# Optimization experiments

Hardware: AMD Instinct MI355X
Metric: run time of the kernel (lower is better)

## Reference

```python
import jax, jax.numpy as jnp
import numpy as np
from jax import lax

B, N, D = 2, 2048, 256
S, DC, E = 16, 4, 2
DI = E * D            # d_inner = 512
DTR = (D + 15) // 16  # dt_rank = 16


def layernorm(x, w, b):
    m = x.mean(-1, keepdims=True)
    v = ((x - m) ** 2).mean(-1, keepdims=True)
    return (x - m) / jnp.sqrt(v + 1e-5) * w + b


def mamba_block(x, in_w, conv_w, conv_b, xproj_w, dt_w, dt_b, A_log, Dp, out_w):
    # x: [B, N, D]
    xz = jnp.einsum('bnd,ed->bne', x, in_w)          # [B,N,2*DI]
    xc, z = jnp.split(xz, 2, axis=-1)
    # depthwise causal conv1d, kernel DC, left-pad DC-1
    xpad = jnp.pad(xc, ((0, 0), (DC - 1, 0), (0, 0)))
    xconv = sum(xpad[:, k:k + N, :] * conv_w[:, k] for k in range(DC)) + conv_b
    xa = jax.nn.silu(xconv)                           # [B,N,DI]
    x_dbl = jnp.einsum('bnd,ed->bne', xa, xproj_w)    # [B,N,DTR+2S]
    dt = x_dbl[..., :DTR]
    Bm = x_dbl[..., DTR:DTR + S]                      # [B,N,S]
    Cm = x_dbl[..., DTR + S:]                         # [B,N,S]
    dt = jax.nn.softplus(jnp.einsum('bnr,dr->bnd', dt, dt_w) + dt_b)  # [B,N,DI]
    A = -jnp.exp(A_log)                               # [DI,S]
    dA = jnp.exp(dt[..., None] * A)                   # [B,N,DI,S]
    dBu = dt[..., None] * Bm[:, :, None, :] * xa[..., None]

    def step(h, inp):
        dA_t, dBu_t, C_t = inp
        h = dA_t * h + dBu_t                          # [B,DI,S]
        y = jnp.einsum('bds,bs->bd', h, C_t)
        return h, y

    h0 = jnp.zeros((x.shape[0], DI, S), dtype=x.dtype)
    _, ys = lax.scan(step, h0, (dA.transpose(1, 0, 2, 3), dBu.transpose(1, 0, 2, 3), Cm.transpose(1, 0, 2)))
    y = ys.transpose(1, 0, 2) + xa * Dp               # skip D*u
    y = y * jax.nn.silu(z)
    return jnp.einsum('bnd,ed->bne', y, out_w)        # [B,N,D]


def stream_fwd(x, nw, nb, in_w, conv_w, conv_b, xproj_w, dt_w, dt_b, A_log, Dp, out_w):
    return x + mamba_block(layernorm(x, nw, nb), in_w, conv_w, conv_b, xproj_w, dt_w, dt_b, A_log, Dp, out_w)


def setup_inputs() -> dict:
    key = jax.random.key(0)
    ks = jax.random.split(key, 24)
    s = 0.02
    inp = {
        'edge_features': jax.random.normal(ks[0], (B, N, D), jnp.float32),
        'blob_features': jax.random.normal(ks[1], (B, N, D), jnp.float32),
        'spectral_features': jax.random.normal(ks[2], (B, N, D), jnp.float32),
        'norm_w': jnp.ones((3, D)),
        'norm_b': jnp.zeros((3, D)),
        'in_w': jax.random.normal(ks[3], (3, 2 * DI, D)) * s,
        'conv_w': jax.random.normal(ks[4], (3, DI, DC)) * s,
        'conv_b': jnp.zeros((3, DI)),
        'xproj_w': jax.random.normal(ks[5], (3, DTR + 2 * S, DI)) * s,
        'dt_w': jax.random.normal(ks[6], (3, DI, DTR)) * s,
        'dt_b': jax.random.uniform(ks[7], (3, DI), minval=-4.0, maxval=-2.0),
        'A_log': jnp.tile(jnp.log(jnp.arange(1, S + 1, dtype=jnp.float32)), (3, DI, 1)),
        'Dp': jnp.ones((3, DI)),
        'out_w': jax.random.normal(ks[8], (3, D, DI)) * s,
        'temperature': jnp.ones((1,)) * 0.1,
        'agg_w1': jax.random.normal(ks[9], (D, 3 * D)) * s,
        'agg_b1': jnp.zeros((D,)),
        'agg_w2': jax.random.normal(ks[10], (3, D)) * s,
        'agg_b2': jnp.zeros((3,)),
        'proj_w': jax.random.normal(ks[11], (D, 3 * D)) * s,
        'proj_b': jnp.zeros((D,)),
    }
    return inp


def reference(edge_features, blob_features, spectral_features, norm_w, norm_b, in_w,
              conv_w, conv_b, xproj_w, dt_w, dt_b, A_log, Dp, out_w, temperature,
              agg_w1, agg_b1, agg_w2, agg_b2, proj_w, proj_b):
    streams = jnp.stack([edge_features, blob_features, spectral_features])  # [3,B,N,D]
    proc = jax.vmap(stream_fwd)(streams, norm_w, norm_b, in_w, conv_w, conv_b,
                                xproj_w, dt_w, dt_b, A_log, Dp, out_w)      # [3,B,N,D]
    edge_p, blob_p, spec_p = proc[0], proc[1], proc[2]
    multi = jnp.concatenate([edge_p, blob_p, spec_p], axis=-1)              # [B,N,3D]
    pooled = multi.mean(axis=1, keepdims=True)                              # [B,1,3D]
    h = jax.nn.gelu(jnp.einsum('bne,de->bnd', pooled, agg_w1) + agg_b1)
    coeffs = jax.nn.softmax(jnp.einsum('bnd,kd->bnk', h, agg_w2) + agg_b2, axis=-1)
    coeffs = jax.nn.softmax(coeffs / (temperature + 1e-6), axis=-1)         # [B,1,3]
    weighted = (coeffs[:, :, 0:1] * edge_p + coeffs[:, :, 1:2] * blob_p +
                coeffs[:, :, 2:3] * spec_p)
    out = jnp.einsum('bne,de->bnd', multi, proj_w) + proj_b + weighted
    return out  # dropout is identity in eval
```

## Files before the change

kernel.cpp:

```cpp
#include <hip/hip_runtime.h>
#include <hip/hip_bf16.h>

#define NB 2
#define NN 2048
#define ND 256
#define NS 16
#define NDC 4
#define NDI 512
#define NDTR 16
#define LCH 32
#define NCH 64

typedef __hip_bfloat16 bf16;
typedef __attribute__((ext_vector_type(8))) __bf16 bf16x8;
typedef __attribute__((ext_vector_type(4))) float f32x4;

__device__ __forceinline__ float b2f(bf16 h) { return __bfloat162float(h); }

__device__ __forceinline__ void dec8(const uint4 u, float w[8]) {
    union { unsigned u; float f; } c;
    c.u = u.x << 16;          w[0] = c.f;
    c.u = u.x & 0xffff0000u;  w[1] = c.f;
    c.u = u.y << 16;          w[2] = c.f;
    c.u = u.y & 0xffff0000u;  w[3] = c.f;
    c.u = u.z << 16;          w[4] = c.f;
    c.u = u.z & 0xffff0000u;  w[5] = c.f;
    c.u = u.w << 16;          w[6] = c.f;
    c.u = u.w & 0xffff0000u;  w[7] = c.f;
}

struct CvtArgs { const void* s[21]; };
__device__ __constant__ const int seg_cum[22] = {
    0, 1048576, 2097152, 3145728, 3146496, 3147264, 3933696, 3939840,
    3941376, 4015104, 4039680, 4041216, 4065792, 4067328, 4460544, 4460545,
    4657153, 4657409, 4658177, 4658180, 4854788, 4855044 };
__device__ __constant__ const int seg_dst[21] = {
    0,        1048576,  2097152,  4847616, 4848384, 3145728, 4841472, 4849152, 4325376,
    4399104,  4850688,  4423680,  4852224, 3932160, 4855056, 4448256, 4853760, 4854016,
    4854784,  4644864,  4854800 };

__global__ __launch_bounds__(256) void k_convert(CvtArgs a, int* __restrict__ flag,
                                                 bf16* __restrict__ dst,
                                                 float* __restrict__ pooled)
{
    int idx = blockIdx.x * 256 + threadIdx.x;
    unsigned v0 = ((const unsigned*)a.s[3])[0];
    int f = ((v0 & 0xFFFFu) == 0u) ? 1 : 0;
    if (idx == 0) flag[0] = f;
    if (idx < 1536) pooled[idx] = 0.0f;
    if (idx >= 4855044) return;
    int seg = 0;
    #pragma unroll
    for (int i = 1; i < 21; i++) if (idx >= seg_cum[i]) seg = i;
    int off = idx - seg_cum[seg];
    bf16 v;
    if (f) v = __float2bfloat16(((const float*)a.s[seg])[off]);
    else   v = ((const bf16*)a.s[seg])[off];
    dst[seg_dst[seg] + off] = v;
}

__global__ __launch_bounds__(256) void k_layernorm(
    const bf16* __restrict__ e, const bf16* __restrict__ bl, const bf16* __restrict__ sp,
    const bf16* __restrict__ nw, const bf16* __restrict__ nb, bf16* __restrict__ xn)
{
    int row = blockIdx.x;
    int sb = row >> 11, n = row & (NN - 1);
    int s = sb >> 1, b = sb & 1;
    const bf16* xin = (s == 0) ? e : ((s == 1) ? bl : sp);
    int t = threadIdx.x;
    float v = b2f(xin[((b << 11) + n) * ND + t]);
    float s1 = v, s2 = v * v;
    #pragma unroll
    for (int m = 1; m < 64; m <<= 1) { s1 += __shfl_xor(s1, m); s2 += __shfl_xor(s2, m); }
    __shared__ float r1[4], r2[4];
    int w = t >> 6;
    if ((t & 63) == 0) { r1[w] = s1; r2[w] = s2; }
    __syncthreads();
    float mean = (r1[0] + r1[1] + r1[2] + r1[3]) * (1.0f / ND);
    float ms   = (r2[0] + r2[1] + r2[2] + r2[3]) * (1.0f / ND);
    float inv = rsqrtf(ms - mean * mean + 1e-5f);
    float wv = b2f(nw[s * ND + t]), bv = b2f(nb[s * ND + t]);
    xn[row * ND + t] = __float2bfloat16((v - mean) * inv * wv + bv);
}

__global__ __launch_bounds__(256) void k_inproj_t(
    const bf16* __restrict__ xn, const bf16* __restrict__ in_w,
    bf16* __restrict__ xc, bf16* __restrict__ z)
{
    __shared__ bf16 As[128 * 72];
    __shared__ bf16 Bs[128 * 72];
    int bid = blockIdx.x;
    int bm = bid >> 3, bn = bid & 7;
    int m0 = bm * 128, e0 = bn * 128;
    int s = m0 >> 12;
    const bf16* W = in_w + (size_t)s * (2 * NDI) * ND;
    int t = threadIdx.x;
    int w = t >> 6, l = t & 63;
    int wm = w >> 1, wn = w & 1;
    int quad = l >> 4, lan = l & 15;
    f32x4 acc[4][4];
    #pragma unroll
    for (int mi = 0; mi < 4; mi++)
        #pragma unroll
        for (int j = 0; j < 4; j++) acc[mi][j] = (f32x4){0.f, 0.f, 0.f, 0.f};
    for (int kc0 = 0; kc0 < 256; kc0 += 64) {
        __syncthreads();
        #pragma unroll
        for (int i = 0; i < 4; i++) {
            int li = i * 256 + t;
            int row = li >> 3, col = (li & 7) * 8;
            *(uint4*)&As[row * 72 + col] =
                *(const uint4*)(xn + (size_t)(m0 + row) * ND + kc0 + col);
        }
        #pragma unroll
        for (int i = 0; i < 4; i++) {
            int li = i * 256 + t;
            int row = li >> 3, col = (li & 7) * 8;
            *(uint4*)&Bs[row * 72 + col] =
                *(const uint4*)(W + (size_t)(e0 + row) * ND + kc0 + col);
        }
        __syncthreads();
        #pragma unroll
        for (int kc = 0; kc < 64; kc += 32) {
            bf16x8 af[4], bf[4];
            #pragma unroll
            for (int mi = 0; mi < 4; mi++)
                af[mi] = *(const bf16x8*)&As[(wm * 64 + mi * 16 + lan) * 72 + kc + quad * 8];
            #pragma unroll
            for (int j = 0; j < 4; j++)
                bf[j] = *(const bf16x8*)&Bs[(wn * 64 + j * 16 + lan) * 72 + kc + quad * 8];
            #pragma unroll
            for (int mi = 0; mi < 4; mi++)
                #pragma unroll
                for (int j = 0; j < 4; j++)
                    acc[mi][j] = __builtin_amdgcn_mfma_f32_16x16x32_bf16(af[mi], bf[j], acc[mi][j], 0, 0, 0);
        }
    }
    #pragma unroll
    for (int mi = 0; mi < 4; mi++) {
        #pragma unroll
        for (int j = 0; j < 4; j++) {
            int e = e0 + wn * 64 + j * 16 + lan;
            bf16* dst = (e < NDI) ? xc : z;
            int ec = e & (NDI - 1);
            #pragma unroll
            for (int r = 0; r < 4; r++) {
                int m = m0 + wm * 64 + mi * 16 + quad * 4 + r;
                dst[(size_t)m * NDI + ec] = __float2bfloat16(acc[mi][j][r]);
            }
        }
    }
}

__global__ __launch_bounds__(256) void k_conv(
    const bf16* __restrict__ xc, const bf16* __restrict__ conv_w,
    const bf16* __restrict__ conv_b, bf16* __restrict__ xa)
{
    int idx = blockIdx.x * 256 + threadIdx.x;
    int d8 = (idx & 63) * 8;
    int rn = idx >> 6;
    int n = rn & (NN - 1);
    int sb = rn >> 11;
    int s = sb >> 1;
    const uint4* cwp = (const uint4*)(conv_w + ((size_t)s * NDI + d8) * NDC);
    float cwf[32];
    dec8(cwp[0], cwf); dec8(cwp[1], cwf + 8); dec8(cwp[2], cwf + 16); dec8(cwp[3], cwf + 24);
    float bias[8];
    dec8(*(const uint4*)(conv_b + (size_t)s * NDI + d8), bias);
    size_t g = (size_t)rn * NDI + d8;
    float xv[4][8];
    #pragma unroll
    for (int tau = 0; tau < 4; tau++) {
        if (n >= tau) dec8(*(const uint4*)(xc + g - (size_t)tau * NDI), xv[tau]);
        else
            #pragma unroll
            for (int j = 0; j < 8; j++) xv[tau][j] = 0.0f;
    }
    union { bf16 h[8]; uint4 u; } o;
    #pragma unroll
    for (int j = 0; j < 8; j++) {
        float a = bias[j];
        #pragma unroll
        for (int k = 0; k < 4; k++) a += cwf[j * 4 + k] * xv[3 - k][j];
        a = a / (1.0f + __expf(-a));
        o.h[j] = __float2bfloat16(a);
    }
    *(uint4*)(xa + g) = o.u;
}

__global__ __launch_bounds__(256) void k_xproj_t(
    const bf16* __restrict__ xa, const bf16* __restrict__ xproj_w,
    float* __restrict__ xpart)
{
    __shared__ bf16 As[64 * 72];
    __shared__ bf16 Bs[48 * 72];
    int bid = blockIdx.x;
    int bm = bid >> 2, ks = bid & 3;
    int m0 = bm * 64;
    int s = m0 >> 12;
    const bf16* W = xproj_w + (size_t)s * 48 * NDI;
    int t = threadIdx.x;
    int w = t >> 6, l = t & 63;
    int quad = l >> 4, lan = l & 15;
    f32x4 acc[3];
    #pragma unroll
    for (int j = 0; j < 3; j++) acc[j] = (f32x4){0.f, 0.f, 0.f, 0.f};
    for (int kc0 = ks * 128; kc0 < ks * 128 + 128; kc0 += 64) {
        __syncthreads();
        #pragma unroll
        for (int i = 0; i < 2; i++) {
            int li = i * 256 + t;
            int row = li >> 3, col = (li & 7) * 8;
            *(uint4*)&As[row * 72 + col] =
                *(const uint4*)(xa + (size_t)(m0 + row) * NDI + kc0 + col);
        }
        {
            int li = t;
            if (li < 384) {
                int row = li >> 3, col = (li & 7) * 8;
                *(uint4*)&Bs[row * 72 + col] =
                    *(const uint4*)(W + (size_t)row * NDI + kc0 + col);
            }
            int li2 = 256 + t;
            if (li2 < 384) {
                int row = li2 >> 3, col = (li2 & 7) * 8;
                *(uint4*)&Bs[row * 72 + col] =
                    *(const uint4*)(W + (size_t)row * NDI + kc0 + col);
            }
        }
        __syncthreads();
        #pragma unroll
        for (int kc = 0; kc < 64; kc += 32) {
            bf16x8 af = *(const bf16x8*)&As[(w * 16 + lan) * 72 + kc + quad * 8];
            #pragma unroll
            for (int j = 0; j < 3; j++) {
                bf16x8 bf = *(const bf16x8*)&Bs[(j * 16 + lan) * 72 + kc + quad * 8];
                acc[j] = __builtin_amdgcn_mfma_f32_16x16x32_bf16(af, bf, acc[j], 0, 0, 0);
            }
        }
    }
    float* dst = xpart + (size_t)ks * (12288 * 48);
    #pragma unroll
    for (int j = 0; j < 3; j++) {
        int e = j * 16 + lan;
        #pragma unroll
        for (int r = 0; r < 4; r++) {
            int m = m0 + w * 16 + quad * 4 + r;
            dst[(size_t)m * 48 + e] = acc[j][r];
        }
    }
}

__global__ __launch_bounds__(256) void k_dt2(
    const float* __restrict__ xpart, const bf16* __restrict__ dt_w,
    const bf16* __restrict__ dt_b, float* __restrict__ xdbl, bf16* __restrict__ dt)
{
    __shared__ float xs[4][48];
    int row0 = blockIdx.x * 4;
    int s = row0 >> 12;
    int t = threadIdx.x;
    if (t < 192) {
        int r = t / 48, e = t % 48;
        size_t base = (size_t)(row0 + r) * 48 + e;
        const size_t seg = (size_t)12288 * 48;
        float v = xpart[base] + xpart[base + seg] + xpart[base + 2 * seg] + xpart[base + 3 * seg];
        xs[r][e] = v;
        if (e >= 16) xdbl[base] = v;
    }
    __syncthreads();
    #pragma unroll
    for (int dd = 0; dd < 2; dd++) {
        int d = t + dd * 256;
        const uint4* wp = (const uint4*)(dt_w + ((size_t)s * NDI + d) * NDTR);
        float w[16]; dec8(wp[0], w); dec8(wp[1], w + 8);
        float bias = b2f(dt_b[s * NDI + d]);
        #pragma unroll
        for (int r = 0; r < 4; r++) {
            float a = bias;
            #pragma unroll
            for (int j = 0; j < 16; j++) a += w[j] * xs[r][j];
            a = (a > 20.0f) ? a : log1pf(__expf(a));
            dt[(size_t)(row0 + r) * NDI + d] = __float2bfloat16(a);
        }
    }
}

__global__ __launch_bounds__(256) void k_scan1(
    const bf16* __restrict__ dt, const bf16* __restrict__ xa,
    const bf16* __restrict__ A_log, const float* __restrict__ xdbl,
    float* __restrict__ Hend, float* __restrict__ Pprod)
{
    __shared__ float Bs[LCH * NS];
    int bid = blockIdx.x;
    int sb = bid / (NCH * 2);
    int rem = bid % (NCH * 2);
    int chunk = rem >> 1, dg = rem & 1;
    int s = sb >> 1;
    int t = threadIdx.x;
    int d = dg * 256 + t;
    int n0 = chunk * LCH;
    size_t rowbase = (size_t)sb * NN;
    if (t < 128) {
        int row = t >> 2, q = t & 3;
        ((float4*)Bs)[t] = ((const float4*)(xdbl + (rowbase + n0 + row) * 48 + 16))[q];
    }
    float A[16];
    {
        const uint4* ap = (const uint4*)(A_log + ((size_t)s * NDI + d) * NS);
        float al[8]; dec8(ap[0], al);
        #pragma unroll
        for (int i = 0; i < 8; i++) A[i] = -__expf(al[i]);
        dec8(ap[1], al);
        #pragma unroll
        for (int i = 0; i < 8; i++) A[8 + i] = -__expf(al[i]);
    }
    __syncthreads();
    float h[16], P[16];
    #pragma unroll
    for (int i = 0; i < 16; i++) { h[i] = 0.0f; P[i] = 1.0f; }
    const bf16* dtp = dt + (rowbase + n0) * NDI + d;
    const bf16* xap = xa + (rowbase + n0) * NDI + d;
    for (int nl = 0; nl < LCH; nl += 4) {
        float dtv[4], xav[4];
        #pragma unroll
        for (int j = 0; j < 4; j++) {
            dtv[j] = b2f(dtp[(size_t)(nl + j) * NDI]);
            xav[j] = b2f(xap[(size_t)(nl + j) * NDI]);
        }
        #pragma unroll
        for (int j = 0; j < 4; j++) {
            float bcom = dtv[j] * xav[j];
            const float4* br = (const float4*)&Bs[(nl + j) * NS];
            float4 b0 = br[0], b1 = br[1], b2 = br[2], b3 = br[3];
            float bv[16] = {b0.x,b0.y,b0.z,b0.w,b1.x,b1.y,b1.z,b1.w,
                            b2.x,b2.y,b2.z,b2.w,b3.x,b3.y,b3.z,b3.w};
            #pragma unroll
            for (int st = 0; st < 16; st++) {
                float dA = __expf(dtv[j] * A[st]);
                h[st] = dA * h[st] + bcom * bv[st];
                P[st] *= dA;
            }
        }
    }
    size_t base = ((size_t)(chunk * 6 + sb) * NS) * NDI + d;
    #pragma unroll
    for (int st = 0; st < 16; st++) {
        Hend[base + (size_t)st * NDI] = h[st];
        Pprod[base + (size_t)st * NDI] = P[st];
    }
}

__global__ __launch_bounds__(256) void k_scomb(float* __restrict__ Hend, const float* __restrict__ Pprod)
{
    int idx = blockIdx.x * 256 + threadIdx.x;
    int sb = idx >> 13;
    int rem = idx & 8191;
    int st = rem >> 9, d = rem & 511;
    float h = 0.0f;
    const size_t stride = (size_t)6 * NS * NDI;
    size_t g = ((size_t)sb * NS + st) * NDI + d;
    #pragma unroll 4
    for (int c = 0; c < NCH; c++) {
        float He = Hend[g], Pp = Pprod[g];
        Hend[g] = h;
        h = He + Pp * h;
        g += stride;
    }
}

__global__ __launch_bounds__(256) void k_scan2(
    const bf16* __restrict__ dt, const bf16* __restrict__ xa, const bf16* __restrict__ z,
    const float* __restrict__ xdbl,
    const bf16* __restrict__ A_log, const bf16* __restrict__ Dp,
    const float* __restrict__ Hstart, bf16* __restrict__ y)
{
    __shared__ float Bs[LCH * NS], Cs[LCH * NS];
    int bid = blockIdx.x;
    int sb = bid / (NCH * 2);
    int rem = bid % (NCH * 2);
    int chunk = rem >> 1, dg = rem & 1;
    int s = sb >> 1;
    int t = threadIdx.x;
    int d = dg * 256 + t;
    int n0 = chunk * LCH;
    size_t rowbase = (size_t)sb * NN;
    if (t < 128) {
        int row = t >> 2, q = t & 3;
        ((float4*)Bs)[t] = ((const float4*)(xdbl + (rowbase + n0 + row) * 48 + 16))[q];
    } else {
        int t2 = t - 128;
        int row = t2 >> 2, q = t2 & 3;
        ((float4*)Cs)[t2] = ((const float4*)(xdbl + (rowbase + n0 + row) * 48 + 32))[q];
    }
    float A[16];
    {
        const uint4* ap = (const uint4*)(A_log + ((size_t)s * NDI + d) * NS);
        float al[8]; dec8(ap[0], al);
        #pragma unroll
        for (int i = 0; i < 8; i++) A[i] = -__expf(al[i]);
        dec8(ap[1], al);
        #pragma unroll
        for (int i = 0; i < 8; i++) A[8 + i] = -__expf(al[i]);
    }
    float Dpv = b2f(Dp[s * NDI + d]);
    float h[16];
    {
        size_t base = ((size_t)(chunk * 6 + sb) * NS) * NDI + d;
        #pragma unroll
        for (int st = 0; st < 16; st++) h[st] = Hstart[base + (size_t)st * NDI];
    }
    __syncthreads();
    const bf16* dtp = dt + (rowbase + n0) * NDI + d;
    const bf16* xap = xa + (rowbase + n0) * NDI + d;
    const bf16* zp  = z  + (rowbase + n0) * NDI + d;
    bf16* yp = y + (rowbase + n0) * NDI + d;
    for (int nl = 0; nl < LCH; nl += 4) {
        float dtv[4], xav[4], zv[4];
        #pragma unroll
        for (int j = 0; j < 4; j++) {
            dtv[j] = b2f(dtp[(size_t)(nl + j) * NDI]);
            xav[j] = b2f(xap[(size_t)(nl + j) * NDI]);
            zv[j]  = b2f(zp [(size_t)(nl + j) * NDI]);
        }
        #pragma unroll
        for (int j = 0; j < 4; j++) {
            float bcom = dtv[j] * xav[j];
            const float4* br = (const float4*)&Bs[(nl + j) * NS];
            const float4* cr = (const float4*)&Cs[(nl + j) * NS];
            float4 b0 = br[0], b1 = br[1], b2 = br[2], b3 = br[3];
            float4 c0 = cr[0], c1 = cr[1], c2 = cr[2], c3 = cr[3];
            float bv[16] = {b0.x,b0.y,b0.z,b0.w,b1.x,b1.y,b1.z,b1.w,
                            b2.x,b2.y,b2.z,b2.w,b3.x,b3.y,b3.z,b3.w};
            float cv[16] = {c0.x,c0.y,c0.z,c0.w,c1.x,c1.y,c1.z,c1.w,
                            c2.x,c2.y,c2.z,c2.w,c3.x,c3.y,c3.z,c3.w};
            float yacc = 0.0f;
            #pragma unroll
            for (int st = 0; st < 16; st++) {
                float dA = __expf(dtv[j] * A[st]);
                h[st] = dA * h[st] + bcom * bv[st];
                yacc += h[st] * cv[st];
            }
            float yv = yacc + xav[j] * Dpv;
            float zz = zv[j];
            yv *= zz / (1.0f + __expf(-zz));
            yp[(size_t)(nl + j) * NDI] = __float2bfloat16(yv);
        }
    }
}

__global__ __launch_bounds__(256) void k_outproj_t(
    const bf16* __restrict__ y, const bf16* __restrict__ out_w,
    const bf16* __restrict__ e_, const bf16* __restrict__ bl, const bf16* __restrict__ sp,
    bf16* __restrict__ proc, float* __restrict__ pooled)
{
    __shared__ bf16 As[128 * 72];
    __shared__ bf16 Bs[64 * 72];
    __shared__ float colsum[64];
    int bid = blockIdx.x;
    int bm = bid >> 2, bn = bid & 3;
    int m0 = bm * 128, e0 = bn * 64;
    int s = m0 >> 12;
    const bf16* W = out_w + (size_t)s * ND * NDI;
    int t = threadIdx.x;
    int w = t >> 6, l = t & 63;
    int quad = l >> 4, lan = l & 15;
    f32x4 acc[2][4];
    #pragma unroll
    for (int mi = 0; mi < 2; mi++)
        #pragma unroll
        for (int j = 0; j < 4; j++) acc[mi][j] = (f32x4){0.f, 0.f, 0.f, 0.f};
    for (int kc0 = 0; kc0 < 512; kc0 += 64) {
        __syncthreads();
        #pragma unroll
        for (int i = 0; i < 4; i++) {
            int li = i * 256 + t;
            int row = li >> 3, col = (li & 7) * 8;
            *(uint4*)&As[row * 72 + col] =
                *(const uint4*)(y + (size_t)(m0 + row) * NDI + kc0 + col);
        }
        #pragma unroll
        for (int i = 0; i < 2; i++) {
            int li = i * 256 + t;
            int row = li >> 3, col = (li & 7) * 8;
            *(uint4*)&Bs[row * 72 + col] =
                *(const uint4*)(W + (size_t)(e0 + row) * NDI + kc0 + col);
        }
        __syncthreads();
        #pragma unroll
        for (int kc = 0; kc < 64; kc += 32) {
            bf16x8 af[2], bf[4];
            #pragma unroll
            for (int mi = 0; mi < 2; mi++)
                af[mi] = *(const bf16x8*)&As[(w * 32 + mi * 16 + lan) * 72 + kc + quad * 8];
            #pragma unroll
            for (int j = 0; j < 4; j++)
                bf[j] = *(const bf16x8*)&Bs[(j * 16 + lan) * 72 + kc + quad * 8];
            #pragma unroll
            for (int mi = 0; mi < 2; mi++)
                #pragma unroll
                for (int j = 0; j < 4; j++)
                    acc[mi][j] = __builtin_amdgcn_mfma_f32_16x16x32_bf16(af[mi], bf[j], acc[mi][j], 0, 0, 0);
        }
    }
    if (t < 64) colsum[t] = 0.0f;
    __syncthreads();
    const bf16* xin = (s == 0) ? e_ : ((s == 1) ? bl : sp);
    int b = (m0 >> 11) & 1;
    #pragma unroll
    for (int mi = 0; mi < 2; mi++) {
        #pragma unroll
        for (int j = 0; j < 4; j++) {
            int e = e0 + j * 16 + lan;
            float ps = 0.0f;
            #pragma unroll
            for (int r = 0; r < 4; r++) {
                int m = m0 + w * 32 + mi * 16 + quad * 4 + r;
                int n = m & (NN - 1);
                float v = acc[mi][j][r] + b2f(xin[((size_t)(b * NN + n)) * ND + e]);
                proc[(size_t)m * ND + e] = __float2bfloat16(v);
                ps += v;
            }
            atomicAdd(&colsum[j * 16 + lan], ps);
        }
    }
    __syncthreads();
    if (t < 64) atomicAdd(&pooled[b * 768 + s * 256 + e0 + t], colsum[t]);
}

__global__ __launch_bounds__(256) void k_coeff(
    const float* __restrict__ pooled,
    const bf16* __restrict__ agg_w1, const bf16* __restrict__ agg_b1,
    const bf16* __restrict__ agg_w2, const bf16* __restrict__ agg_b2,
    const bf16* __restrict__ temp, float* __restrict__ coeffs)
{
    __shared__ float hb[256];
    __shared__ float lg[3];
    int t = threadIdx.x;
    for (int b = 0; b < NB; b++) {
        float dot = 0.0f;
        const uint4* wp = (const uint4*)(agg_w1 + (size_t)t * 768);
        for (int k8 = 0; k8 < 96; k8++) {
            float w[8]; dec8(wp[k8], w);
            const float* pp = pooled + b * 768 + k8 * 8;
            #pragma unroll
            for (int j = 0; j < 8; j++) dot += w[j] * pp[j];
        }
        float x = b2f(agg_b1[t]) + dot * (1.0f / NN);
        float inner = 0.7978845608028654f * (x + 0.044715f * x * x * x);
        hb[t] = 0.5f * x * (1.0f + tanhf(inner));
        __syncthreads();
        if (t < 3) {
            float l = b2f(agg_b2[t]);
            const bf16* w2 = agg_w2 + t * 256;
            for (int d2 = 0; d2 < 256; d2++) l += b2f(w2[d2]) * hb[d2];
            lg[t] = l;
        }
        __syncthreads();
        if (t == 0) {
            float m = fmaxf(lg[0], fmaxf(lg[1], lg[2]));
            float e0 = __expf(lg[0] - m), e1 = __expf(lg[1] - m), e2 = __expf(lg[2] - m);
            float iS = 1.0f / (e0 + e1 + e2);
            float c0 = e0 * iS, c1 = e1 * iS, c2 = e2 * iS;
            float tt = b2f(temp[0]) + 1e-6f;
            float m2 = fmaxf(c0, fmaxf(c1, c2)) / tt;
            e0 = __expf(c0 / tt - m2); e1 = __expf(c1 / tt - m2); e2 = __expf(c2 / tt - m2);
            iS = 1.0f / (e0 + e1 + e2);
            coeffs[b * 3 + 0] = e0 * iS;
            coeffs[b * 3 + 1] = e1 * iS;
            coeffs[b * 3 + 2] = e2 * iS;
        }
        __syncthreads();
    }
}

__global__ __launch_bounds__(256) void k_final_t(
    const bf16* __restrict__ proc, const bf16* __restrict__ proj_w,
    const bf16* __restrict__ proj_b, const float* __restrict__ coeffs,
    const int* __restrict__ flag, void* __restrict__ out)
{
    __shared__ bf16 As[128 * 72];
    __shared__ bf16 Bs[64 * 72];
    int bid = blockIdx.x;
    int bm = bid >> 2, bn = bid & 3;
    int m0 = bm * 128, e0 = bn * 64;
    int b = m0 >> 11;
    int nbase = m0 & (NN - 1);
    int t = threadIdx.x;
    int w = t >> 6, l = t & 63;
    int quad = l >> 4, lan = l & 15;
    f32x4 acc[2][4];
    #pragma unroll
    for (int mi = 0; mi < 2; mi++)
        #pragma unroll
        for (int j = 0; j < 4; j++) acc[mi][j] = (f32x4){0.f, 0.f, 0.f, 0.f};
    for (int kc0 = 0; kc0 < 768; kc0 += 64) {
        int sA = kc0 >> 8, kd0 = kc0 & 255;
        const bf16* Asrc = proc + ((size_t)(sA * NB + b) * NN + nbase) * ND + kd0;
        __syncthreads();
        #pragma unroll
        for (int i = 0; i < 4; i++) {
            int li = i * 256 + t;
            int row = li >> 3, col = (li & 7) * 8;
            *(uint4*)&As[row * 72 + col] = *(const uint4*)(Asrc + (size_t)row * ND + col);
        }
        #pragma unroll
        for (int i = 0; i < 2; i++) {
            int li = i * 256 + t;
            int row = li >> 3, col = (li & 7) * 8;
            *(uint4*)&Bs[row * 72 + col] =
                *(const uint4*)(proj_w + (size_t)(e0 + row) * 768 + kc0 + col);
        }
        __syncthreads();
        #pragma unroll
        for (int kc = 0; kc < 64; kc += 32) {
            bf16x8 af[2], bf[4];
            #pragma unroll
            for (int mi = 0; mi < 2; mi++)
                af[mi] = *(const bf16x8*)&As[(w * 32 + mi * 16 + lan) * 72 + kc + quad * 8];
            #pragma unroll
            for (int j = 0; j < 4; j++)
                bf[j] = *(const bf16x8*)&Bs[(j * 16 + lan) * 72 + kc + quad * 8];
            #pragma unroll
            for (int mi = 0; mi < 2; mi++)
                #pragma unroll
                for (int j = 0; j < 4; j++)
                    acc[mi][j] = __builtin_amdgcn_mfma_f32_16x16x32_bf16(af[mi], bf[j], acc[mi][j], 0, 0, 0);
        }
    }
    float c0 = coeffs[b * 3], c1 = coeffs[b * 3 + 1], c2 = coeffs[b * 3 + 2];
    int f = flag[0];
    #pragma unroll
    for (int mi = 0; mi < 2; mi++) {
        #pragma unroll
        for (int j = 0; j < 4; j++) {
            int e = e0 + j * 16 + lan;
            float pb = b2f(proj_b[e]);
            #pragma unroll
            for (int r = 0; r < 4; r++) {
                int m = m0 + w * 32 + mi * 16 + quad * 4 + r;
                int n = m & (NN - 1);
                size_t pbase = ((size_t)b * NN + n) * ND + e;
                float wres = c0 * b2f(proc[pbase])
                           + c1 * b2f(proc[pbase + (size_t)1 * NB * NN * ND])
                           + c2 * b2f(proc[pbase + (size_t)2 * NB * NN * ND]);
                float v = acc[mi][j][r] + pb + wres;
                if (f) ((float*)out)[(size_t)m * ND + e] = v;
                else   ((bf16*)out)[(size_t)m * ND + e] = __float2bfloat16(v);
            }
        }
    }
}

extern "C" void kernel_launch(void* const* d_in, const int* in_sizes, int n_in,
                              void* d_out, int out_size, void* d_ws, size_t ws_size,
                              hipStream_t stream)
{
    char* w8 = (char*)d_ws;
    int*   flagp   = (int*)(w8);
    bf16*  cvt     = (bf16*)(w8 + 16);
    bf16*  xn      = (bf16*)(w8 + 9710160);
    bf16*  xcb     = (bf16*)(w8 + 16001616);
    bf16*  zb      = (bf16*)(w8 + 28584528);
    bf16*  xab     = (bf16*)(w8 + 41167440);
    bf16*  dtb     = (bf16*)(w8 + 53750352);
    float* xdblb   = (float*)(w8 + 66333264);
    float* pooledb = (float*)(w8 + 68692560);
    float* coeffsb = (float*)(w8 + 68698704);
    float* Hendb   = (float*)(w8 + 68698736);
    float* Pprodb  = (float*)(w8 + 81281648);
    float* xpartb  = (float*)(w8 + 93864560);
    bf16*  procb   = xn;

    const bf16* c_edge   = cvt + 0;
    const bf16* c_blob   = cvt + 1048576;
    const bf16* c_spec   = cvt + 2097152;
    const bf16* c_inw    = cvt + 3145728;
    const bf16* c_outw   = cvt + 3932160;
    const bf16* c_xpw    = cvt + 4325376;
    const bf16* c_dtw    = cvt + 4399104;
    const bf16* c_alog   = cvt + 4423680;
    const bf16* c_agg1   = cvt + 4448256;
    const bf16* c_prjw   = cvt + 4644864;
    const bf16* c_convw  = cvt + 4841472;
    const bf16* c_nrmw   = cvt + 4847616;
    const bf16* c_nrmb   = cvt + 4848384;
    const bf16* c_convb  = cvt + 4849152;
    const bf16* c_dtb    = cvt + 4850688;
    const bf16* c_dp     = cvt + 4852224;
    const bf16* c_agb1   = cvt + 4853760;
    const bf16* c_agw2   = cvt + 4854016;
    const bf16* c_agb2   = cvt + 4854784;
    const bf16* c_prjb   = cvt + 4854800;
    const bf16* c_temp   = cvt + 4855056;

    CvtArgs ca;
    for (int i = 0; i < 21; i++) ca.s[i] = d_in[i];
    k_convert<<<(4855044 + 255) / 256, 256, 0, stream>>>(ca, flagp, cvt, pooledb);

    k_layernorm<<<6 * NN, 256, 0, stream>>>(c_edge, c_blob, c_spec, c_nrmw, c_nrmb, xn);
    k_inproj_t<<<96 * 8, 256, 0, stream>>>(xn, c_inw, xcb, zb);
    k_conv<<<6 * NN * NDI / 8 / 256, 256, 0, stream>>>(xcb, c_convw, c_convb, xab);
    k_xproj_t<<<192 * 4, 256, 0, stream>>>(xab, c_xpw, xpartb);
    k_dt2<<<3072, 256, 0, stream>>>(xpartb, c_dtw, c_dtb, xdblb, dtb);
    k_scan1<<<6 * NCH * 2, 256, 0, stream>>>(dtb, xab, c_alog, xdblb, Hendb, Pprodb);
    k_scomb<<<192, 256, 0, stream>>>(Hendb, Pprodb);
    k_scan2<<<6 * NCH * 2, 256, 0, stream>>>(dtb, xab, zb, xdblb, c_alog, c_dp, Hendb, xcb);
    k_outproj_t<<<96 * 4, 256, 0, stream>>>(xcb, c_outw, c_edge, c_blob, c_spec, procb, pooledb);
    k_coeff<<<1, 256, 0, stream>>>(pooledb, c_agg1, c_agb1, c_agw2, c_agb2, c_temp, coeffsb);
    k_final_t<<<32 * 4, 256, 0, stream>>>(procb, c_prjw, c_prjb, coeffsb, flagp, d_out);
}
```

Before: 337.3 us.

## Fuse input conversion into layernorm, stage scan inputs in LDS, fold coeff into final

The three large feature tensors are no longer converted in the convert kernel. Layernorm now reads the raw inputs, writes the bf16 copy itself and reads the norm weights raw. The scan kernels stage dt, xa and z chunks in shared memory with coalesced 16-byte loads instead of strided per-thread loads. The single-block coeff kernel is folded into every block of the final GEMM, which removes one launch but makes each of the 128 blocks recompute the small MLP.

```diff
diff --git a/kernel.cpp b/kernel.cpp
--- a/kernel.cpp
+++ b/kernel.cpp
@@ -43,15 +43,16 @@
                                                  bf16* __restrict__ dst,
                                                  float* __restrict__ pooled)
 {
-    int idx = blockIdx.x * 256 + threadIdx.x;
+    int idx0 = blockIdx.x * 256 + threadIdx.x;
     unsigned v0 = ((const unsigned*)a.s[3])[0];
     int f = ((v0 & 0xFFFFu) == 0u) ? 1 : 0;
-    if (idx == 0) flag[0] = f;
-    if (idx < 1536) pooled[idx] = 0.0f;
+    if (idx0 == 0) flag[0] = f;
+    if (idx0 < 1536) pooled[idx0] = 0.0f;
+    int idx = idx0 + 3145728;
     if (idx >= 4855044) return;
-    int seg = 0;
-    #pragma unroll
-    for (int i = 1; i < 21; i++) if (idx >= seg_cum[i]) seg = i;
+    int seg = 3;
+    #pragma unroll
+    for (int i = 4; i < 21; i++) if (idx >= seg_cum[i]) seg = i;
     int off = idx - seg_cum[seg];
     bf16 v;
     if (f) v = __float2bfloat16(((const float*)a.s[seg])[off]);
@@ -59,16 +60,22 @@
     dst[seg_dst[seg] + off] = v;
 }
 
-__global__ __launch_bounds__(256) void k_layernorm(
-    const bf16* __restrict__ e, const bf16* __restrict__ bl, const bf16* __restrict__ sp,
-    const bf16* __restrict__ nw, const bf16* __restrict__ nb, bf16* __restrict__ xn)
+__global__ __launch_bounds__(256) void k_ln(
+    const void* __restrict__ e, const void* __restrict__ bl, const void* __restrict__ sp,
+    const void* __restrict__ nw_raw, const void* __restrict__ nb_raw,
+    bf16* __restrict__ cvt_in,
+    bf16* __restrict__ xn)
 {
     int row = blockIdx.x;
     int sb = row >> 11, n = row & (NN - 1);
     int s = sb >> 1, b = sb & 1;
-    const bf16* xin = (s == 0) ? e : ((s == 1) ? bl : sp);
     int t = threadIdx.x;
-    float v = b2f(xin[((b << 11) + n) * ND + t]);
+    unsigned v0 = ((const unsigned*)nw_raw)[0];
+    int f = ((v0 & 0xFFFFu) == 0u);
+    const void* xin = (s == 0) ? e : ((s == 1) ? bl : sp);
+    size_t gi = ((size_t)(b << 11) + n) * ND + t;
+    float v = f ? ((const float*)xin)[gi] : b2f(((const bf16*)xin)[gi]);
+    cvt_in[(size_t)s * 1048576 + gi] = __float2bfloat16(v);
     float s1 = v, s2 = v * v;
     #pragma unroll
     for (int m = 1; m < 64; m <<= 1) { s1 += __shfl_xor(s1, m); s2 += __shfl_xor(s2, m); }
@@ -79,8 +86,9 @@
     float mean = (r1[0] + r1[1] + r1[2] + r1[3]) * (1.0f / ND);
     float ms   = (r2[0] + r2[1] + r2[2] + r2[3]) * (1.0f / ND);
     float inv = rsqrtf(ms - mean * mean + 1e-5f);
-    float wv = b2f(nw[s * ND + t]), bv = b2f(nb[s * ND + t]);
-    xn[row * ND + t] = __float2bfloat16((v - mean) * inv * wv + bv);
+    float wv = f ? ((const float*)nw_raw)[s * ND + t] : b2f(((const bf16*)nw_raw)[s * ND + t]);
+    float bv = f ? ((const float*)nb_raw)[s * ND + t] : b2f(((const bf16*)nb_raw)[s * ND + t]);
+    xn[(size_t)row * ND + t] = __float2bfloat16((v - mean) * inv * wv + bv);
 }
 
 __global__ __launch_bounds__(256) void k_inproj_t(
@@ -290,6 +298,8 @@
     const bf16* __restrict__ A_log, const float* __restrict__ xdbl,
     float* __restrict__ Hend, float* __restrict__ Pprod)
 {
+    __shared__ bf16 dts[LCH * 256];
+    __shared__ bf16 xas[LCH * 256];
     __shared__ float Bs[LCH * NS];
     int bid = blockIdx.x;
     int sb = bid / (NCH * 2);
@@ -300,6 +310,15 @@
     int d = dg * 256 + t;
     int n0 = chunk * LCH;
     size_t rowbase = (size_t)sb * NN;
+    const bf16* dtg = dt + (rowbase + n0) * NDI + dg * 256;
+    const bf16* xag = xa + (rowbase + n0) * NDI + dg * 256;
+    #pragma unroll
+    for (int i = 0; i < 4; i++) {
+        int li = i * 256 + t;
+        int row = li >> 5, q = li & 31;
+        ((uint4*)dts)[li] = *(const uint4*)(dtg + (size_t)row * NDI + q * 8);
+        ((uint4*)xas)[li] = *(const uint4*)(xag + (size_t)row * NDI + q * 8);
+    }
     if (t < 128) {
         int row = t >> 2, q = t & 3;
         ((float4*)Bs)[t] = ((const float4*)(xdbl + (rowbase + n0 + row) * 48 + 16))[q];
@@ -318,28 +337,20 @@
     float h[16], P[16];
     #pragma unroll
     for (int i = 0; i < 16; i++) { h[i] = 0.0f; P[i] = 1.0f; }
-    const bf16* dtp = dt + (rowbase + n0) * NDI + d;
-    const bf16* xap = xa + (rowbase + n0) * NDI + d;
-    for (int nl = 0; nl < LCH; nl += 4) {
-        float dtv[4], xav[4];
-        #pragma unroll
-        for (int j = 0; j < 4; j++) {
-            dtv[j] = b2f(dtp[(size_t)(nl + j) * NDI]);
-            xav[j] = b2f(xap[(size_t)(nl + j) * NDI]);
-        }
-        #pragma unroll
-        for (int j = 0; j < 4; j++) {
-            float bcom = dtv[j] * xav[j];
-            const float4* br = (const float4*)&Bs[(nl + j) * NS];
-            float4 b0 = br[0], b1 = br[1], b2 = br[2], b3 = br[3];
-            float bv[16] = {b0.x,b0.y,b0.z,b0.w,b1.x,b1.y,b1.z,b1.w,
-                            b2.x,b2.y,b2.z,b2.w,b3.x,b3.y,b3.z,b3.w};
-            #pragma unroll
-            for (int st = 0; st < 16; st++) {
-                float dA = __expf(dtv[j] * A[st]);
-                h[st] = dA * h[st] + bcom * bv[st];
-                P[st] *= dA;
-            }
+    #pragma unroll 4
+    for (int nl = 0; nl < LCH; nl++) {
+        float dtv = b2f(dts[nl * 256 + t]);
+        float xav = b2f(xas[nl * 256 + t]);
+        float bcom = dtv * xav;
+        const float4* br = (const float4*)&Bs[nl * NS];
+        float4 b0 = br[0], b1 = br[1], b2 = br[2], b3 = br[3];
+        float bv[16] = {b0.x,b0.y,b0.z,b0.w,b1.x,b1.y,b1.z,b1.w,
+                        b2.x,b2.y,b2.z,b2.w,b3.x,b3.y,b3.z,b3.w};
+        #pragma unroll
+        for (int st = 0; st < 16; st++) {
+            float dA = __expf(dtv * A[st]);
+            h[st] = dA * h[st] + bcom * bv[st];
+            P[st] *= dA;
         }
     }
     size_t base = ((size_t)(chunk * 6 + sb) * NS) * NDI + d;
@@ -374,6 +385,9 @@
     const bf16* __restrict__ A_log, const bf16* __restrict__ Dp,
     const float* __restrict__ Hstart, bf16* __restrict__ y)
 {
+    __shared__ bf16 dts[LCH * 256];
+    __shared__ bf16 xas[LCH * 256];
+    __shared__ bf16 zs[LCH * 256];
     __shared__ float Bs[LCH * NS], Cs[LCH * NS];
     int bid = blockIdx.x;
     int sb = bid / (NCH * 2);
@@ -384,6 +398,17 @@
     int d = dg * 256 + t;
     int n0 = chunk * LCH;
     size_t rowbase = (size_t)sb * NN;
+    const bf16* dtg = dt + (rowbase + n0) * NDI + dg * 256;
+    const bf16* xag = xa + (rowbase + n0) * NDI + dg * 256;
+    const bf16* zg  = z  + (rowbase + n0) * NDI + dg * 256;
+    #pragma unroll
+    for (int i = 0; i < 4; i++) {
+        int li = i * 256 + t;
+        int row = li >> 5, q = li & 31;
+        ((uint4*)dts)[li] = *(const uint4*)(dtg + (size_t)row * NDI + q * 8);
+        ((uint4*)xas)[li] = *(const uint4*)(xag + (size_t)row * NDI + q * 8);
+        ((uint4*)zs)[li]  = *(const uint4*)(zg  + (size_t)row * NDI + q * 8);
+    }
     if (t < 128) {
         int row = t >> 2, q = t & 3;
         ((float4*)Bs)[t] = ((const float4*)(xdbl + (rowbase + n0 + row) * 48 + 16))[q];
@@ -410,41 +435,31 @@
         for (int st = 0; st < 16; st++) h[st] = Hstart[base + (size_t)st * NDI];
     }
     __syncthreads();
-    const bf16* dtp = dt + (rowbase + n0) * NDI + d;
-    const bf16* xap = xa + (rowbase + n0) * NDI + d;
-    const bf16* zp  = z  + (rowbase + n0) * NDI + d;
     bf16* yp = y + (rowbase + n0) * NDI + d;
-    for (int nl = 0; nl < LCH; nl += 4) {
-        float dtv[4], xav[4], zv[4];
-        #pragma unroll
-        for (int j = 0; j < 4; j++) {
-            dtv[j] = b2f(dtp[(size_t)(nl + j) * NDI]);
-            xav[j] = b2f(xap[(size_t)(nl + j) * NDI]);
-            zv[j]  = b2f(zp [(size_t)(nl + j) * NDI]);
-        }
-        #pragma unroll
-        for (int j = 0; j < 4; j++) {
-            float bcom = dtv[j] * xav[j];
-            const float4* br = (const float4*)&Bs[(nl + j) * NS];
-            const float4* cr = (const float4*)&Cs[(nl + j) * NS];
-            float4 b0 = br[0], b1 = br[1], b2 = br[2], b3 = br[3];
-            float4 c0 = cr[0], c1 = cr[1], c2 = cr[2], c3 = cr[3];
-            float bv[16] = {b0.x,b0.y,b0.z,b0.w,b1.x,b1.y,b1.z,b1.w,
-                            b2.x,b2.y,b2.z,b2.w,b3.x,b3.y,b3.z,b3.w};
-            float cv[16] = {c0.x,c0.y,c0.z,c0.w,c1.x,c1.y,c1.z,c1.w,
-                            c2.x,c2.y,c2.z,c2.w,c3.x,c3.y,c3.z,c3.w};
-            float yacc = 0.0f;
-            #pragma unroll
-            for (int st = 0; st < 16; st++) {
-                float dA = __expf(dtv[j] * A[st]);
-                h[st] = dA * h[st] + bcom * bv[st];
-                yacc += h[st] * cv[st];
-            }
-            float yv = yacc + xav[j] * Dpv;
-            float zz = zv[j];
-            yv *= zz / (1.0f + __expf(-zz));
-            yp[(size_t)(nl + j) * NDI] = __float2bfloat16(yv);
-        }
+    #pragma unroll 4
+    for (int nl = 0; nl < LCH; nl++) {
+        float dtv = b2f(dts[nl * 256 + t]);
+        float xav = b2f(xas[nl * 256 + t]);
+        float zz  = b2f(zs[nl * 256 + t]);
+        float bcom = dtv * xav;
+        const float4* br = (const float4*)&Bs[nl * NS];
+        const float4* cr = (const float4*)&Cs[nl * NS];
+        float4 b0 = br[0], b1 = br[1], b2 = br[2], b3 = br[3];
+        float4 c0 = cr[0], c1 = cr[1], c2 = cr[2], c3 = cr[3];
+        float bv[16] = {b0.x,b0.y,b0.z,b0.w,b1.x,b1.y,b1.z,b1.w,
+                        b2.x,b2.y,b2.z,b2.w,b3.x,b3.y,b3.z,b3.w};
+        float cv[16] = {c0.x,c0.y,c0.z,c0.w,c1.x,c1.y,c1.z,c1.w,
+                        c2.x,c2.y,c2.z,c2.w,c3.x,c3.y,c3.z,c3.w};
+        float yacc = 0.0f;
+        #pragma unroll
+        for (int st = 0; st < 16; st++) {
+            float dA = __expf(dtv * A[st]);
+            h[st] = dA * h[st] + bcom * bv[st];
+            yacc += h[st] * cv[st];
+        }
+        float yv = yacc + xav * Dpv;
+        yv *= zz / (1.0f + __expf(-zz));
+        yp[(size_t)nl * NDI] = __float2bfloat16(yv);
     }
 }
 
@@ -527,59 +542,19 @@
     if (t < 64) atomicAdd(&pooled[b * 768 + s * 256 + e0 + t], colsum[t]);
 }
 
-__global__ __launch_bounds__(256) void k_coeff(
-    const float* __restrict__ pooled,
+__global__ __launch_bounds__(256) void k_final_t(
+    const bf16* __restrict__ proc, const bf16* __restrict__ proj_w,
+    const bf16* __restrict__ proj_b, const float* __restrict__ pooled,
     const bf16* __restrict__ agg_w1, const bf16* __restrict__ agg_b1,
     const bf16* __restrict__ agg_w2, const bf16* __restrict__ agg_b2,
-    const bf16* __restrict__ temp, float* __restrict__ coeffs)
-{
+    const bf16* __restrict__ temp,
+    const int* __restrict__ flag, void* __restrict__ out)
+{
+    __shared__ bf16 As[128 * 72];
+    __shared__ bf16 Bs[64 * 72];
     __shared__ float hb[256];
     __shared__ float lg[3];
-    int t = threadIdx.x;
-    for (int b = 0; b < NB; b++) {
-        float dot = 0.0f;
-        const uint4* wp = (const uint4*)(agg_w1 + (size_t)t * 768);
-        for (int k8 = 0; k8 < 96; k8++) {
-            float w[8]; dec8(wp[k8], w);
-            const float* pp = pooled + b * 768 + k8 * 8;
-            #pragma unroll
-            for (int j = 0; j < 8; j++) dot += w[j] * pp[j];
-        }
-        float x = b2f(agg_b1[t]) + dot * (1.0f / NN);
-        float inner = 0.7978845608028654f * (x + 0.044715f * x * x * x);
-        hb[t] = 0.5f * x * (1.0f + tanhf(inner));
-        __syncthreads();
-        if (t < 3) {
-            float l = b2f(agg_b2[t]);
-            const bf16* w2 = agg_w2 + t * 256;
-            for (int d2 = 0; d2 < 256; d2++) l += b2f(w2[d2]) * hb[d2];
-            lg[t] = l;
-        }
-        __syncthreads();
-        if (t == 0) {
-            float m = fmaxf(lg[0], fmaxf(lg[1], lg[2]));
-            float e0 = __expf(lg[0] - m), e1 = __expf(lg[1] - m), e2 = __expf(lg[2] - m);
-            float iS = 1.0f / (e0 + e1 + e2);
-            float c0 = e0 * iS, c1 = e1 * iS, c2 = e2 * iS;
-            float tt = b2f(temp[0]) + 1e-6f;
-            float m2 = fmaxf(c0, fmaxf(c1, c2)) / tt;
-            e0 = __expf(c0 / tt - m2); e1 = __expf(c1 / tt - m2); e2 = __expf(c2 / tt - m2);
-            iS = 1.0f / (e0 + e1 + e2);
-            coeffs[b * 3 + 0] = e0 * iS;
-            coeffs[b * 3 + 1] = e1 * iS;
-            coeffs[b * 3 + 2] = e2 * iS;
-        }
-        __syncthreads();
-    }
-}
-
-__global__ __launch_bounds__(256) void k_final_t(
-    const bf16* __restrict__ proc, const bf16* __restrict__ proj_w,
-    const bf16* __restrict__ proj_b, const float* __restrict__ coeffs,
-    const int* __restrict__ flag, void* __restrict__ out)
-{
-    __shared__ bf16 As[128 * 72];
-    __shared__ bf16 Bs[64 * 72];
+    __shared__ float cf[3];
     int bid = blockIdx.x;
     int bm = bid >> 2, bn = bid & 3;
     int m0 = bm * 128, e0 = bn * 64;
@@ -588,6 +563,38 @@
     int t = threadIdx.x;
     int w = t >> 6, l = t & 63;
     int quad = l >> 4, lan = l & 15;
+    {
+        float dot = 0.0f;
+        const uint4* wp = (const uint4*)(agg_w1 + (size_t)t * 768);
+        for (int k8 = 0; k8 < 96; k8++) {
+            float wv[8]; dec8(wp[k8], wv);
+            const float* pp = pooled + b * 768 + k8 * 8;
+            #pragma unroll
+            for (int j = 0; j < 8; j++) dot += wv[j] * pp[j];
+        }
+        float x = b2f(agg_b1[t]) + dot * (1.0f / NN);
+        float inner = 0.7978845608028654f * (x + 0.044715f * x * x * x);
+        hb[t] = 0.5f * x * (1.0f + tanhf(inner));
+        __syncthreads();
+        if (t < 3) {
+            float ll = b2f(agg_b2[t]);
+            const bf16* w2 = agg_w2 + t * 256;
+            for (int d2 = 0; d2 < 256; d2++) ll += b2f(w2[d2]) * hb[d2];
+            lg[t] = ll;
+        }
+        __syncthreads();
+        if (t == 0) {
+            float m = fmaxf(lg[0], fmaxf(lg[1], lg[2]));
+            float e0f = __expf(lg[0] - m), e1 = __expf(lg[1] - m), e2 = __expf(lg[2] - m);
+            float iS = 1.0f / (e0f + e1 + e2);
+            float c0 = e0f * iS, c1 = e1 * iS, c2 = e2 * iS;
+            float tt = b2f(temp[0]) + 1e-6f;
+            float m2 = fmaxf(c0, fmaxf(c1, c2)) / tt;
+            e0f = __expf(c0 / tt - m2); e1 = __expf(c1 / tt - m2); e2 = __expf(c2 / tt - m2);
+            iS = 1.0f / (e0f + e1 + e2);
+            cf[0] = e0f * iS; cf[1] = e1 * iS; cf[2] = e2 * iS;
+        }
+    }
     f32x4 acc[2][4];
     #pragma unroll
     for (int mi = 0; mi < 2; mi++)
@@ -627,7 +634,7 @@
                     acc[mi][j] = __builtin_amdgcn_mfma_f32_16x16x32_bf16(af[mi], bf[j], acc[mi][j], 0, 0, 0);
         }
     }
-    float c0 = coeffs[b * 3], c1 = coeffs[b * 3 + 1], c2 = coeffs[b * 3 + 2];
+    float c0 = cf[0], c1 = cf[1], c2 = cf[2];
     int f = flag[0];
     #pragma unroll
     for (int mi = 0; mi < 2; mi++) {
@@ -665,7 +672,6 @@
     bf16*  dtb     = (bf16*)(w8 + 53750352);
     float* xdblb   = (float*)(w8 + 66333264);
     float* pooledb = (float*)(w8 + 68692560);
-    float* coeffsb = (float*)(w8 + 68698704);
     float* Hendb   = (float*)(w8 + 68698736);
     float* Pprodb  = (float*)(w8 + 81281648);
     float* xpartb  = (float*)(w8 + 93864560);
@@ -682,8 +688,6 @@
     const bf16* c_agg1   = cvt + 4448256;
     const bf16* c_prjw   = cvt + 4644864;
     const bf16* c_convw  = cvt + 4841472;
-    const bf16* c_nrmw   = cvt + 4847616;
-    const bf16* c_nrmb   = cvt + 4848384;
     const bf16* c_convb  = cvt + 4849152;
     const bf16* c_dtb    = cvt + 4850688;
     const bf16* c_dp     = cvt + 4852224;
@@ -695,9 +699,9 @@
 
     CvtArgs ca;
     for (int i = 0; i < 21; i++) ca.s[i] = d_in[i];
-    k_convert<<<(4855044 + 255) / 256, 256, 0, stream>>>(ca, flagp, cvt, pooledb);
-
-    k_layernorm<<<6 * NN, 256, 0, stream>>>(c_edge, c_blob, c_spec, c_nrmw, c_nrmb, xn);
+    k_convert<<<(1709316 + 255) / 256, 256, 0, stream>>>(ca, flagp, cvt, pooledb);
+    k_ln<<<6 * NN, 256, 0, stream>>>(d_in[0], d_in[1], d_in[2], d_in[3], d_in[4],
+                                     cvt, xn);
     k_inproj_t<<<96 * 8, 256, 0, stream>>>(xn, c_inw, xcb, zb);
     k_conv<<<6 * NN * NDI / 8 / 256, 256, 0, stream>>>(xcb, c_convw, c_convb, xab);
     k_xproj_t<<<192 * 4, 256, 0, stream>>>(xab, c_xpw, xpartb);
@@ -706,6 +710,7 @@
     k_scomb<<<192, 256, 0, stream>>>(Hendb, Pprodb);
     k_scan2<<<6 * NCH * 2, 256, 0, stream>>>(dtb, xab, zb, xdblb, c_alog, c_dp, Hendb, xcb);
     k_outproj_t<<<96 * 4, 256, 0, stream>>>(xcb, c_outw, c_edge, c_blob, c_spec, procb, pooledb);
-    k_coeff<<<1, 256, 0, stream>>>(pooledb, c_agg1, c_agb1, c_agw2, c_agb2, c_temp, coeffsb);
-    k_final_t<<<32 * 4, 256, 0, stream>>>(procb, c_prjw, c_prjb, coeffsb, flagp, d_out);
-}
+    k_final_t<<<32 * 4, 256, 0, stream>>>(procb, c_prjw, c_prjb, pooledb,
+                                          c_agg1, c_agb1, c_agw2, c_agb2, c_temp,
+                                          flagp, d_out);
+}
```

Result: faster. 327.4 us (-2.9%).
